# Kernel optimization log

Hardware: AMD Instinct MI355X
Metric: run time of the kernel (lower is better)

The kernel has to match this reference:

```python
import jax, jax.numpy as jnp
import numpy as np

NUM_INPUTS = 4096
K = 64
BATCH = 16384


def setup_inputs() -> dict:
    key = jax.random.key(0)
    X = jax.random.normal(key, (BATCH, NUM_INPUTS), dtype=jnp.float32)
    return {"X": X}


def reference(X):
    # Per-row (1 - k/n) quantile of |X| (linear interpolation, matching
    # torch.quantile default), then soft-threshold preserving sign.
    q = 1.0 - K / NUM_INPUTS
    X_abs = jnp.abs(X)
    Q = jnp.quantile(X_abs, q, axis=1, method="linear")  # [batch]
    X_trunc = jnp.maximum(X_abs - Q[:, None], 0.0)
    return jnp.sign(X) * X_trunc
```

## Files before the change

### kernel.cpp

```cpp
#include <hip/hip_runtime.h>
#include <cstdint>

constexpr int NCOLS   = 4096;
constexpr int THREADS = 256;
constexpr int EPT     = 16;
constexpr int CAP     = 256;

__global__ __launch_bounds__(THREADS) void topk_sparsify(
    const float* __restrict__ X, float* __restrict__ out)
{
    const int row  = blockIdx.x;
    const int t    = threadIdx.x;
    const int wave = t >> 6;
    const int lane = t & 63;

    __shared__ uint32_t wsum[4];
    __shared__ float    fsum[4];
    __shared__ uint32_t cand[CAP];

    const float4* __restrict__ x4 =
        reinterpret_cast<const float4*>(X + (size_t)row * NCOLS);
    float4* __restrict__ o4 = reinterpret_cast<float4*>(out + (size_t)row * NCOLS);

    uint32_t a[EPT];
    uint32_t sbits = 0;
    float ss = 0.0f;
#pragma unroll
    for (int i = 0; i < 4; ++i) {
        float4 v = x4[t + THREADS * i];
        uint32_t u0 = __float_as_uint(v.x), u1 = __float_as_uint(v.y);
        uint32_t u2 = __float_as_uint(v.z), u3 = __float_as_uint(v.w);
        a[4*i+0] = u0 & 0x7FFFFFFFu;  a[4*i+1] = u1 & 0x7FFFFFFFu;
        a[4*i+2] = u2 & 0x7FFFFFFFu;  a[4*i+3] = u3 & 0x7FFFFFFFu;
        sbits |= (u0 >> 31) << (4*i+0);
        sbits |= (u1 >> 31) << (4*i+1);
        sbits |= (u2 >> 31) << (4*i+2);
        sbits |= (u3 >> 31) << (4*i+3);
        ss = fmaf(v.x, v.x, ss); ss = fmaf(v.y, v.y, ss);
        ss = fmaf(v.z, v.z, ss); ss = fmaf(v.w, v.w, ss);
    }

#pragma unroll
    for (int off = 32; off >= 1; off >>= 1) ss += __shfl_xor(ss, off, 64);
    if (lane == 0) fsum[wave] = ss;
    __syncthreads();
    const float sigma = sqrtf(fsum[0] + fsum[1] + fsum[2] + fsum[3]) * (1.0f / 64.0f);

    float T = 2.1f * sigma;
    uint32_t tb = 0, C = 0, myc = 0;
    bool ok = false;
    for (int it = 0; it < 16; ++it) {
        tb  = __float_as_uint(T);
        myc = 0;
#pragma unroll
        for (int i = 0; i < EPT; ++i) myc += (a[i] > tb) ? 1u : 0u;
        uint32_t c = myc;
#pragma unroll
        for (int off = 32; off >= 1; off >>= 1) c += __shfl_xor(c, off, 64);
        __syncthreads();
        if (lane == 0) wsum[wave] = c;
        __syncthreads();
        C = wsum[0] + wsum[1] + wsum[2] + wsum[3];
        if (C >= 65u && C <= (uint32_t)CAP) { ok = true; break; }
        T = (C < 65u) ? T * 0.70f : T * 1.35f;
    }

    uint32_t b65;
    if (ok) {
        uint32_t pre = myc;
#pragma unroll
        for (int off = 1; off < 64; off <<= 1) {
            uint32_t v = __shfl_up(pre, off, 64);
            if (lane >= off) pre += v;
        }
        uint32_t wtot = __shfl(pre, 63, 64);
        __syncthreads();
        if (lane == 0) wsum[wave] = wtot;
        __syncthreads();
        uint32_t base = 0;
#pragma unroll
        for (int w = 0; w < 4; ++w) base += (w < wave) ? wsum[w] : 0u;
        uint32_t o = base + pre - myc;
#pragma unroll
        for (int i = 0; i < EPT; ++i)
            if (a[i] > tb) cand[o++] = a[i];
        __syncthreads();

        uint32_t r0 = (lane        < (int)C) ? cand[lane      ] : 0u;
        uint32_t r1 = (lane + 64   < (int)C) ? cand[lane +  64] : 0u;
        uint32_t r2 = (lane + 128  < (int)C) ? cand[lane + 128] : 0u;
        uint32_t r3 = (lane + 192  < (int)C) ? cand[lane + 192] : 0u;

        uint32_t mx = max(max(r0, r1), max(r2, r3));
#pragma unroll
        for (int off = 32; off >= 1; off >>= 1)
            mx = max(mx, (uint32_t)__shfl_xor(mx, off, 64));

        uint32_t lo = tb + 1u, hi = mx;
        while (lo < hi) {
            uint32_t mid = lo + ((hi - lo) >> 1);
            uint32_t c = ((r0 > mid) ? 1u : 0u) + ((r1 > mid) ? 1u : 0u) +
                         ((r2 > mid) ? 1u : 0u) + ((r3 > mid) ? 1u : 0u);
#pragma unroll
            for (int off = 32; off >= 1; off >>= 1) c += __shfl_xor(c, off, 64);
            if (c < 65u) hi = mid; else lo = mid + 1u;
        }
        b65 = lo;
    } else {
        uint32_t lo = 0u, hi = 0x7F800000u;
        while (lo < hi) {
            uint32_t mid = lo + ((hi - lo) >> 1);
            uint32_t c = 0;
#pragma unroll
            for (int i = 0; i < EPT; ++i) c += (a[i] > mid) ? 1u : 0u;
#pragma unroll
            for (int off = 32; off >= 1; off >>= 1) c += __shfl_xor(c, off, 64);
            __syncthreads();
            if (lane == 0) wsum[wave] = c;
            __syncthreads();
            uint32_t tot = wsum[0] + wsum[1] + wsum[2] + wsum[3];
            if (tot < 65u) hi = mid; else lo = mid + 1u;
        }
        b65 = lo;
    }

    uint32_t cnt = 0, mn = 0xFFFFFFFFu;
#pragma unroll
    for (int i = 0; i < EPT; ++i) {
        bool g = a[i] > b65;
        cnt += g ? 1u : 0u;
        mn = min(mn, g ? a[i] : 0xFFFFFFFFu);
    }
#pragma unroll
    for (int off = 32; off >= 1; off >>= 1) {
        cnt += __shfl_xor(cnt, off, 64);
        mn = min(mn, (uint32_t)__shfl_xor(mn, off, 64));
    }
    __syncthreads();
    if (lane == 0) { wsum[wave] = cnt; fsum[wave] = __uint_as_float(mn); }
    __syncthreads();
    const uint32_t Ct = wsum[0] + wsum[1] + wsum[2] + wsum[3];
    const uint32_t M  = min(min(__float_as_uint(fsum[0]), __float_as_uint(fsum[1])),
                            min(__float_as_uint(fsum[2]), __float_as_uint(fsum[3])));
    const float v65 = __uint_as_float(b65);
    const float v64 = (Ct == 64u) ? __uint_as_float(M) : v65;
    const float Q = fmaf(0.015625f, v64 - v65, v65);

#pragma unroll
    for (int i = 0; i < 4; ++i) {
        float r[4];
#pragma unroll
        for (int j = 0; j < 4; ++j) {
            const int idx = 4*i + j;
            float mag = fmaxf(__uint_as_float(a[idx]) - Q, 0.0f);
            uint32_t bits = __float_as_uint(mag) | (((sbits >> idx) & 1u) << 31);
            r[j] = __uint_as_float(bits);
        }
        o4[t + THREADS * i] = make_float4(r[0], r[1], r[2], r[3]);
    }
}

extern "C" void kernel_launch(void* const* d_in, const int* in_sizes, int n_in,
                              void* d_out, int out_size, void* d_ws, size_t ws_size,
                              hipStream_t stream) {
    const float* X   = (const float*)d_in[0];
    float*       out = (float*)d_out;
    const int rows = in_sizes[0] / NCOLS;
    topk_sparsify<<<rows, THREADS, 0, stream>>>(X, out);
}
```

Measured before the change: 447.1 us.

## Replace shuffle reductions with ballot/popcount counting and streamline selection passes

```diff
diff --git a/kernel.cpp b/kernel.cpp
--- a/kernel.cpp
+++ b/kernel.cpp
@@ -5,6 +5,13 @@
 constexpr int THREADS = 256;
 constexpr int EPT     = 16;
 constexpr int CAP     = 256;
+
+typedef float floatx4 __attribute__((ext_vector_type(4)));
+
+__device__ __forceinline__ uint32_t mbcnt64(uint64_t m) {
+    uint32_t c = __builtin_amdgcn_mbcnt_lo((uint32_t)m, 0u);
+    return __builtin_amdgcn_mbcnt_hi((uint32_t)(m >> 32), c);
+}
 
 __global__ __launch_bounds__(THREADS) void topk_sparsify(
     const float* __restrict__ X, float* __restrict__ out)
@@ -16,18 +23,19 @@
 
     __shared__ uint32_t wsum[4];
     __shared__ float    fsum[4];
+    __shared__ uint32_t wmn[4];
     __shared__ uint32_t cand[CAP];
 
-    const float4* __restrict__ x4 =
-        reinterpret_cast<const float4*>(X + (size_t)row * NCOLS);
-    float4* __restrict__ o4 = reinterpret_cast<float4*>(out + (size_t)row * NCOLS);
+    const floatx4* __restrict__ x4 =
+        reinterpret_cast<const floatx4*>(X + (size_t)row * NCOLS);
+    floatx4* __restrict__ o4 = reinterpret_cast<floatx4*>(out + (size_t)row * NCOLS);
 
     uint32_t a[EPT];
     uint32_t sbits = 0;
     float ss = 0.0f;
 #pragma unroll
     for (int i = 0; i < 4; ++i) {
-        float4 v = x4[t + THREADS * i];
+        floatx4 v = x4[t + THREADS * i];
         uint32_t u0 = __float_as_uint(v.x), u1 = __float_as_uint(v.y);
         uint32_t u2 = __float_as_uint(v.z), u3 = __float_as_uint(v.w);
         a[4*i+0] = u0 & 0x7FFFFFFFu;  a[4*i+1] = u1 & 0x7FFFFFFFu;
@@ -46,117 +54,111 @@
     __syncthreads();
     const float sigma = sqrtf(fsum[0] + fsum[1] + fsum[2] + fsum[3]) * (1.0f / 64.0f);
 
-    float T = 2.1f * sigma;
-    uint32_t tb = 0, C = 0, myc = 0;
+    float T = 2.12f * sigma;
+    uint32_t tb = 0, C = 0;
     bool ok = false;
-    for (int it = 0; it < 16; ++it) {
-        tb  = __float_as_uint(T);
-        myc = 0;
+    for (int it = 0; it < 12; ++it) {
+        tb = __float_as_uint(T);
+        uint32_t cw = 0;
 #pragma unroll
-        for (int i = 0; i < EPT; ++i) myc += (a[i] > tb) ? 1u : 0u;
-        uint32_t c = myc;
-#pragma unroll
-        for (int off = 32; off >= 1; off >>= 1) c += __shfl_xor(c, off, 64);
-        __syncthreads();
-        if (lane == 0) wsum[wave] = c;
+        for (int i = 0; i < EPT; ++i)
+            cw += (uint32_t)__popcll(__ballot(a[i] > tb));
+        if (lane == 0) wsum[wave] = cw;
         __syncthreads();
         C = wsum[0] + wsum[1] + wsum[2] + wsum[3];
         if (C >= 65u && C <= (uint32_t)CAP) { ok = true; break; }
-        T = (C < 65u) ? T * 0.70f : T * 1.35f;
+        __syncthreads();
+        T = (C < 65u) ? T * 0.82f : T * 1.25f;
     }
 
-    uint32_t b65;
+    uint32_t b65, Ct, M;
     if (ok) {
-        uint32_t pre = myc;
-#pragma unroll
-        for (int off = 1; off < 64; off <<= 1) {
-            uint32_t v = __shfl_up(pre, off, 64);
-            if (lane >= off) pre += v;
-        }
-        uint32_t wtot = __shfl(pre, 63, 64);
-        __syncthreads();
-        if (lane == 0) wsum[wave] = wtot;
-        __syncthreads();
         uint32_t base = 0;
 #pragma unroll
         for (int w = 0; w < 4; ++w) base += (w < wave) ? wsum[w] : 0u;
-        uint32_t o = base + pre - myc;
 #pragma unroll
-        for (int i = 0; i < EPT; ++i)
-            if (a[i] > tb) cand[o++] = a[i];
+        for (int i = 0; i < EPT; ++i) {
+            uint64_t m = __ballot(a[i] > tb);
+            if (a[i] > tb) cand[base + mbcnt64(m)] = a[i];
+            base += (uint32_t)__popcll(m);
+        }
         __syncthreads();
 
-        uint32_t r0 = (lane        < (int)C) ? cand[lane      ] : 0u;
-        uint32_t r1 = (lane + 64   < (int)C) ? cand[lane +  64] : 0u;
-        uint32_t r2 = (lane + 128  < (int)C) ? cand[lane + 128] : 0u;
-        uint32_t r3 = (lane + 192  < (int)C) ? cand[lane + 192] : 0u;
+        uint32_t r0 = (lane       < (int)C) ? cand[lane      ] : 0u;
+        uint32_t r1 = (lane + 64  < (int)C) ? cand[lane +  64] : 0u;
+        uint32_t r2 = (lane + 128 < (int)C) ? cand[lane + 128] : 0u;
+        uint32_t r3 = (lane + 192 < (int)C) ? cand[lane + 192] : 0u;
 
-        uint32_t mx = max(max(r0, r1), max(r2, r3));
-#pragma unroll
-        for (int off = 32; off >= 1; off >>= 1)
-            mx = max(mx, (uint32_t)__shfl_xor(mx, off, 64));
-
-        uint32_t lo = tb + 1u, hi = mx;
+        uint32_t lo = tb + 1u, hi = 0x7F800000u;
         while (lo < hi) {
             uint32_t mid = lo + ((hi - lo) >> 1);
-            uint32_t c = ((r0 > mid) ? 1u : 0u) + ((r1 > mid) ? 1u : 0u) +
-                         ((r2 > mid) ? 1u : 0u) + ((r3 > mid) ? 1u : 0u);
-#pragma unroll
-            for (int off = 32; off >= 1; off >>= 1) c += __shfl_xor(c, off, 64);
+            uint32_t c = (uint32_t)(__popcll(__ballot(r0 > mid)) +
+                                    __popcll(__ballot(r1 > mid)) +
+                                    __popcll(__ballot(r2 > mid)) +
+                                    __popcll(__ballot(r3 > mid)));
             if (c < 65u) hi = mid; else lo = mid + 1u;
         }
         b65 = lo;
+
+        Ct = (uint32_t)(__popcll(__ballot(r0 > b65)) +
+                        __popcll(__ballot(r1 > b65)) +
+                        __popcll(__ballot(r2 > b65)) +
+                        __popcll(__ballot(r3 > b65)));
+        uint32_t mn = 0xFFFFFFFFu;
+        mn = min(mn, (r0 > b65) ? r0 : 0xFFFFFFFFu);
+        mn = min(mn, (r1 > b65) ? r1 : 0xFFFFFFFFu);
+        mn = min(mn, (r2 > b65) ? r2 : 0xFFFFFFFFu);
+        mn = min(mn, (r3 > b65) ? r3 : 0xFFFFFFFFu);
+#pragma unroll
+        for (int off = 32; off >= 1; off >>= 1)
+            mn = min(mn, (uint32_t)__shfl_xor(mn, off, 64));
+        M = mn;
     } else {
         uint32_t lo = 0u, hi = 0x7F800000u;
         while (lo < hi) {
             uint32_t mid = lo + ((hi - lo) >> 1);
-            uint32_t c = 0;
+            uint32_t cw = 0;
 #pragma unroll
-            for (int i = 0; i < EPT; ++i) c += (a[i] > mid) ? 1u : 0u;
-#pragma unroll
-            for (int off = 32; off >= 1; off >>= 1) c += __shfl_xor(c, off, 64);
-            __syncthreads();
-            if (lane == 0) wsum[wave] = c;
+            for (int i = 0; i < EPT; ++i)
+                cw += (uint32_t)__popcll(__ballot(a[i] > mid));
+            if (lane == 0) wsum[wave] = cw;
             __syncthreads();
             uint32_t tot = wsum[0] + wsum[1] + wsum[2] + wsum[3];
+            __syncthreads();
             if (tot < 65u) hi = mid; else lo = mid + 1u;
         }
         b65 = lo;
+
+        uint32_t cw = 0, mn = 0xFFFFFFFFu;
+#pragma unroll
+        for (int i = 0; i < EPT; ++i) {
+            cw += (uint32_t)__popcll(__ballot(a[i] > b65));
+            mn = min(mn, (a[i] > b65) ? a[i] : 0xFFFFFFFFu);
+        }
+#pragma unroll
+        for (int off = 32; off >= 1; off >>= 1)
+            mn = min(mn, (uint32_t)__shfl_xor(mn, off, 64));
+        if (lane == 0) { wsum[wave] = cw; wmn[wave] = mn; }
+        __syncthreads();
+        Ct = wsum[0] + wsum[1] + wsum[2] + wsum[3];
+        M  = min(min(wmn[0], wmn[1]), min(wmn[2], wmn[3]));
     }
 
-    uint32_t cnt = 0, mn = 0xFFFFFFFFu;
-#pragma unroll
-    for (int i = 0; i < EPT; ++i) {
-        bool g = a[i] > b65;
-        cnt += g ? 1u : 0u;
-        mn = min(mn, g ? a[i] : 0xFFFFFFFFu);
-    }
-#pragma unroll
-    for (int off = 32; off >= 1; off >>= 1) {
-        cnt += __shfl_xor(cnt, off, 64);
-        mn = min(mn, (uint32_t)__shfl_xor(mn, off, 64));
-    }
-    __syncthreads();
-    if (lane == 0) { wsum[wave] = cnt; fsum[wave] = __uint_as_float(mn); }
-    __syncthreads();
-    const uint32_t Ct = wsum[0] + wsum[1] + wsum[2] + wsum[3];
-    const uint32_t M  = min(min(__float_as_uint(fsum[0]), __float_as_uint(fsum[1])),
-                            min(__float_as_uint(fsum[2]), __float_as_uint(fsum[3])));
     const float v65 = __uint_as_float(b65);
     const float v64 = (Ct == 64u) ? __uint_as_float(M) : v65;
     const float Q = fmaf(0.015625f, v64 - v65, v65);
 
 #pragma unroll
     for (int i = 0; i < 4; ++i) {
-        float r[4];
+        floatx4 f;
 #pragma unroll
         for (int j = 0; j < 4; ++j) {
             const int idx = 4*i + j;
             float mag = fmaxf(__uint_as_float(a[idx]) - Q, 0.0f);
             uint32_t bits = __float_as_uint(mag) | (((sbits >> idx) & 1u) << 31);
-            r[j] = __uint_as_float(bits);
+            f[j] = __uint_as_float(bits);
         }
-        o4[t + THREADS * i] = make_float4(r[0], r[1], r[2], r[3]);
+        __builtin_nontemporal_store(f, &o4[t + THREADS * i]);
     }
 }
 
```

Measured after the change: 441.9 us. About the same (-1.2%).
